# Kernel optimization log

Hardware: AMD Instinct MI355X
Metric: run time of the kernel (lower is better)

The kernel has to match this reference:

```python
import jax, jax.numpy as jnp
import numpy as np

L, B, H, P = 2048, 32, 128, 256  # seq len, batch, feature dim, state dim


def setup_inputs() -> dict:
    key = jax.random.key(0)
    ks = jax.random.split(key, 9)
    log_min, log_max = np.log(0.001), np.log(0.1)
    return {
        "input_sequences": jax.random.normal(ks[0], (L, B, H), dtype=jnp.float32),
        # -Lambda.real of a HiPPO block diag is positive; emulate with small positive values
        "log_Lambda_real": jnp.log(0.5 + jax.random.uniform(ks[1], (P,), dtype=jnp.float32)),
        "Lambda_imag": jax.random.normal(ks[2], (P,), dtype=jnp.float32) * 3.0,
        "B_tilde_r": jax.random.normal(ks[3], (P, H), dtype=jnp.float32) * (0.5 / np.sqrt(H)),
        "B_tilde_i": jax.random.normal(ks[4], (P, H), dtype=jnp.float32) * (0.5 / np.sqrt(H)),
        "C_tilde_r": jax.random.normal(ks[5], (H, P), dtype=jnp.float32) * (0.5 / np.sqrt(P)),
        "C_tilde_i": jax.random.normal(ks[6], (H, P), dtype=jnp.float32) * (0.5 / np.sqrt(P)),
        "D": jax.random.normal(ks[7], (H,), dtype=jnp.float32),
        "log_Delta": log_min + (log_max - log_min) * jax.random.uniform(ks[8], (P,), dtype=jnp.float32),
    }


def reference(input_sequences, log_Lambda_real, Lambda_imag, B_tilde_r, B_tilde_i,
              C_tilde_r, C_tilde_i, D, log_Delta):
    l = input_sequences.shape[0]
    u = input_sequences.astype(jnp.complex64)  # (L,B,H)
    lam = (-jnp.exp(log_Lambda_real) + 1j * Lambda_imag).astype(jnp.complex64)  # (P,)
    log_Lambda_bar = lam * jnp.exp(log_Delta).astype(jnp.complex64)  # scale_factor=1.0
    # kernel[t, p] = exp(log_Lambda_bar[p] * (L-1-t))  -> (L,P)
    steps = jnp.arange(l - 1, -1, -1, dtype=jnp.float32).astype(jnp.complex64)
    kernel = jnp.exp(steps[:, None] * log_Lambda_bar[None, :])
    B_tilde = (B_tilde_r + 1j * B_tilde_i).astype(jnp.complex64)  # (P,H)
    B_bar = ((kernel[-2] - 1.0) / lam)[:, None] * B_tilde  # (P,H)
    Bu = jnp.einsum('nm,lbm->lbn', B_bar, u)  # (L,B,P)
    # FFT convolution: flipped kernel is exp(log_Lambda_bar * t)
    kff = jnp.fft.fft(kernel[::-1], n=2 * l, axis=0)[:, None, :]  # (2L,1,P)
    buff = jnp.fft.fft(Bu, n=2 * l, axis=0)  # (2L,B,P)
    o = jnp.fft.ifft(kff * buff, axis=0)[:l]  # (L,B,P)
    xs = jnp.einsum('hn,lbn->lbh', (C_tilde_r + 1j * C_tilde_i).astype(jnp.complex64), o)
    xs = xs + (D * input_sequences).astype(jnp.complex64)
    return jnp.real(xs)
```

## Files before the change

kernel.cpp:

```cpp
#include <hip/hip_runtime.h>
#include <math.h>

#define SL 2048
#define NB 32
#define NH 128
#define NP 256
#define NP2 512

typedef short bf16x8 __attribute__((ext_vector_type(8)));
typedef float f32x4  __attribute__((ext_vector_type(4)));

static __device__ __forceinline__ unsigned short f2bf(float x) {
    unsigned u = __float_as_uint(x);
    return (unsigned short)((u + 0x7fffu + ((u >> 16) & 1u)) >> 16);
}
static __device__ __forceinline__ float bf2f(unsigned short h) {
    return __uint_as_float(((unsigned)h) << 16);
}
static __device__ __forceinline__ void discretize(
    const float* __restrict__ logLr, const float* __restrict__ Lim,
    const float* __restrict__ logDt, int p, float& wr, float& wi)
{
    const float Lr = expf(logLr[p]);
    const float dt = expf(logDt[p]);
    const float ew = expf(-Lr * dt);
    const float ang = Lim[p] * dt;
    wr = ew * cosf(ang); wi = ew * sinf(ang);
}

__global__ __launch_bounds__(256) void k0(
    const float* __restrict__ logLr, const float* __restrict__ Lim,
    const float* __restrict__ logDt,
    const float* __restrict__ Br, const float* __restrict__ Bi,
    const float* __restrict__ Cr, const float* __restrict__ Ci,
    unsigned short* __restrict__ BhatF, unsigned short* __restrict__ ChatF)
{
    const int tid = blockIdx.x * 256 + threadIdx.x;
    const int p = tid >> 7, h = tid & 127;
    float wr, wi; discretize(logLr, Lim, logDt, p, wr, wi);
    const float Lr = expf(logLr[p]), li = Lim[p];
    const float nr = wr - 1.0f, ni = wi;
    const float den = Lr * Lr + li * li;
    const float fr = (-nr * Lr + ni * li) / den;
    const float fi = (-ni * Lr - nr * li) / den;
    const float br = Br[p * NH + h], bi = Bi[p * NH + h];
    BhatF[((size_t)(h >> 5) << 14) + ((2 * p)     << 5) + (h & 31)] = f2bf(fr * br - fi * bi);
    BhatF[((size_t)(h >> 5) << 14) + ((2 * p + 1) << 5) + (h & 31)] = f2bf(fr * bi + fi * br);
    const int col0 = 2 * p, col1 = 2 * p + 1;
    ChatF[((size_t)(col0 >> 5) << 12) + (h << 5) + (col0 & 31)] = f2bf(Cr[h * NP + p]);
    ChatF[((size_t)(col1 >> 5) << 12) + (h << 5) + (col1 & 31)] = f2bf(-Ci[h * NP + p]);
}

__global__ __launch_bounds__(256, 4) void gA(
    const float* __restrict__ u, const unsigned short* __restrict__ BhatF,
    const float* __restrict__ logLr, const float* __restrict__ Lim,
    const float* __restrict__ logDt, float2* __restrict__ part)
{
    __shared__ unsigned short us[32][136];
    __shared__ unsigned xs[32 * 129];

    const int m  = blockIdx.x;
    const int ph = blockIdx.y;
    const int b  = blockIdx.z;
    const int tid = threadIdx.x;
    const int w = tid >> 6, lane = tid & 63;
    const int q = lane >> 4, c = lane & 15;
    const int pbase = ph * 256 + w * 64;
    const int l0 = m * 32;

    {
        const int lrow = tid >> 3;
        const int hcol = (tid & 7) * 16;
        const float* up = u + (size_t)(l0 + lrow) * (NB * NH) + b * NH + hcol;
        float4 a = *(const float4*)(up + 0);
        float4 d = *(const float4*)(up + 4);
        float4 e = *(const float4*)(up + 8);
        float4 g = *(const float4*)(up + 12);
        uint4 w0, w1;
        w0.x = (unsigned)f2bf(a.x) | ((unsigned)f2bf(a.y) << 16);
        w0.y = (unsigned)f2bf(a.z) | ((unsigned)f2bf(a.w) << 16);
        w0.z = (unsigned)f2bf(d.x) | ((unsigned)f2bf(d.y) << 16);
        w0.w = (unsigned)f2bf(d.z) | ((unsigned)f2bf(d.w) << 16);
        w1.x = (unsigned)f2bf(e.x) | ((unsigned)f2bf(e.y) << 16);
        w1.y = (unsigned)f2bf(e.z) | ((unsigned)f2bf(e.w) << 16);
        w1.z = (unsigned)f2bf(g.x) | ((unsigned)f2bf(g.y) << 16);
        w1.w = (unsigned)f2bf(g.z) | ((unsigned)f2bf(g.w) << 16);
        *(uint4*)&us[lrow][hcol + 0] = w0;
        *(uint4*)&us[lrow][hcol + 8] = w1;
    }
    __syncthreads();

    f32x4 acc[4][2];
    #pragma unroll
    for (int mt = 0; mt < 4; ++mt)
        #pragma unroll
        for (int nt = 0; nt < 2; ++nt) acc[mt][nt] = (f32x4){0.f, 0.f, 0.f, 0.f};

    #pragma unroll
    for (int kk = 0; kk < 4; ++kk) {
        bf16x8 af[4];
        #pragma unroll
        for (int mt = 0; mt < 4; ++mt)
            af[mt] = *(const bf16x8*)(BhatF + ((size_t)kk << 14)
                                      + ((pbase + 16 * mt + c) << 5) + 8 * q);
        bf16x8 bfr[2];
        #pragma unroll
        for (int nt = 0; nt < 2; ++nt)
            bfr[nt] = *(const bf16x8*)&us[16 * nt + c][kk * 32 + 8 * q];
        #pragma unroll
        for (int mt = 0; mt < 4; ++mt)
            #pragma unroll
            for (int nt = 0; nt < 2; ++nt)
                acc[mt][nt] = __builtin_amdgcn_mfma_f32_16x16x32_bf16(
                    af[mt], bfr[nt], acc[mt][nt], 0, 0, 0);
    }

    #pragma unroll
    for (int mt = 0; mt < 4; ++mt)
        #pragma unroll
        for (int nt = 0; nt < 2; ++nt) {
            const int rw  = 16 * nt + c;
            const int ppl = w * 64 + 16 * mt + 4 * q;
            ushort4 st;
            st.x = f2bf(acc[mt][nt][0]); st.y = f2bf(acc[mt][nt][1]);
            st.z = f2bf(acc[mt][nt][2]); st.w = f2bf(acc[mt][nt][3]);
            const int col = (ppl >> 1);
            xs[rw * 129 + col]     = (unsigned)st.x | ((unsigned)st.y << 16);
            xs[rw * 129 + col + 1] = (unsigned)st.z | ((unsigned)st.w << 16);
        }
    __syncthreads();

    if (tid < 128) {
        float wr, wi; discretize(logLr, Lim, logDt, ph * 128 + tid, wr, wi);
        float sr = 0.f, si = 0.f;
        unsigned va[8], vb[8];
        #pragma unroll
        for (int j = 0; j < 8; ++j) va[j] = xs[j * 129 + tid];
        #pragma unroll
        for (int k8 = 0; k8 < 4; ++k8) {
            if (k8 < 3) {
                #pragma unroll
                for (int j = 0; j < 8; ++j) vb[j] = xs[((k8 + 1) * 8 + j) * 129 + tid];
            }
            #pragma unroll
            for (int j = 0; j < 8; ++j) {
                const float xr = bf2f((unsigned short)(va[j] & 0xffffu));
                const float xi = bf2f((unsigned short)(va[j] >> 16));
                const float tr = wr * sr - wi * si + xr;
                const float ti = wr * si + wi * sr + xi;
                sr = tr; si = ti;
            }
            #pragma unroll
            for (int j = 0; j < 8; ++j) va[j] = vb[j];
        }
        part[((size_t)b * 64 + m) * NP + ph * 128 + tid] = make_float2(sr, si);
    }
}

__global__ __launch_bounds__(256) void s2(
    float2* __restrict__ part, const float* __restrict__ logLr,
    const float* __restrict__ Lim, const float* __restrict__ logDt)
{
    const int b = blockIdx.x, p = threadIdx.x;
    float wr, wi; discretize(logLr, Lim, logDt, p, wr, wi);
    float Wr = wr, Wi = wi;
    #pragma unroll
    for (int t = 0; t < 5; ++t) { const float r = Wr * Wr - Wi * Wi; Wi = 2.f * Wr * Wi; Wr = r; }
    const size_t base = (size_t)b * 64 * NP + p;
    float sr = 0.f, si = 0.f;
    float2 va[8], vb[8];
    #pragma unroll
    for (int j = 0; j < 8; ++j) va[j] = part[base + (size_t)j * NP];
    #pragma unroll
    for (int k8 = 0; k8 < 8; ++k8) {
        if (k8 < 7) {
            #pragma unroll
            for (int j = 0; j < 8; ++j)
                vb[j] = part[base + (size_t)((k8 + 1) * 8 + j) * NP];
        }
        #pragma unroll
        for (int j = 0; j < 8; ++j) {
            part[base + (size_t)(k8 * 8 + j) * NP] = make_float2(sr, si);
            const float tr = Wr * sr - Wi * si + va[j].x;
            const float ti = Wr * si + Wi * sr + va[j].y;
            sr = tr; si = ti;
        }
        #pragma unroll
        for (int j = 0; j < 8; ++j) va[j] = vb[j];
    }
}

__global__ __launch_bounds__(256, 4) void gF(
    const float* __restrict__ u, const unsigned short* __restrict__ BhatF,
    const unsigned short* __restrict__ ChatF,
    const float* __restrict__ logLr, const float* __restrict__ Lim,
    const float* __restrict__ logDt, const float2* __restrict__ Ent,
    const float* __restrict__ Dv, float* __restrict__ out)
{
    __shared__ unsigned short us[32][136];
    __shared__ char osb[16384];

    const int m = blockIdx.x, b = blockIdx.y;
    const int tid = threadIdx.x;
    const int w = tid >> 6, lane = tid & 63;
    const int q = lane >> 4, c = lane & 15;
    const int hbase = w * 32;
    const int l0 = m * 32;

    {
        const int lrow = tid >> 3;
        const int hcol = (tid & 7) * 16;
        const float* up = u + (size_t)(l0 + lrow) * (NB * NH) + b * NH + hcol;
        float4 a = *(const float4*)(up + 0);
        float4 d = *(const float4*)(up + 4);
        float4 e = *(const float4*)(up + 8);
        float4 g = *(const float4*)(up + 12);
        uint4 w0, w1;
        w0.x = (unsigned)f2bf(a.x) | ((unsigned)f2bf(a.y) << 16);
        w0.y = (unsigned)f2bf(a.z) | ((unsigned)f2bf(a.w) << 16);
        w0.z = (unsigned)f2bf(d.x) | ((unsigned)f2bf(d.y) << 16);
        w0.w = (unsigned)f2bf(d.z) | ((unsigned)f2bf(d.w) << 16);
        w1.x = (unsigned)f2bf(e.x) | ((unsigned)f2bf(e.y) << 16);
        w1.y = (unsigned)f2bf(e.z) | ((unsigned)f2bf(e.w) << 16);
        w1.z = (unsigned)f2bf(g.x) | ((unsigned)f2bf(g.y) << 16);
        w1.w = (unsigned)f2bf(g.z) | ((unsigned)f2bf(g.w) << 16);
        *(uint4*)&us[lrow][hcol + 0] = w0;
        *(uint4*)&us[lrow][hcol + 8] = w1;
    }
    __syncthreads();

    f32x4 acc2[2][2];
    #pragma unroll
    for (int mt = 0; mt < 2; ++mt)
        #pragma unroll
        for (int nt = 0; nt < 2; ++nt) acc2[mt][nt] = (f32x4){0.f, 0.f, 0.f, 0.f};

    #pragma unroll 1
    for (int half = 0; half < 2; ++half) {
        const int pbase = half * 256 + w * 64;
        f32x4 acc[4][2];
        #pragma unroll
        for (int mt = 0; mt < 4; ++mt)
            #pragma unroll
            for (int nt = 0; nt < 2; ++nt) acc[mt][nt] = (f32x4){0.f, 0.f, 0.f, 0.f};
        #pragma unroll
        for (int kk = 0; kk < 4; ++kk) {
            bf16x8 af[4];
            #pragma unroll
            for (int mt = 0; mt < 4; ++mt)
                af[mt] = *(const bf16x8*)(BhatF + ((size_t)kk << 14)
                                          + ((pbase + 16 * mt + c) << 5) + 8 * q);
            bf16x8 bfr[2];
            #pragma unroll
            for (int nt = 0; nt < 2; ++nt)
                bfr[nt] = *(const bf16x8*)&us[16 * nt + c][kk * 32 + 8 * q];
            #pragma unroll
            for (int mt = 0; mt < 4; ++mt)
                #pragma unroll
                for (int nt = 0; nt < 2; ++nt)
                    acc[mt][nt] = __builtin_amdgcn_mfma_f32_16x16x32_bf16(
                        af[mt], bfr[nt], acc[mt][nt], 0, 0, 0);
        }

        #pragma unroll
        for (int mt = 0; mt < 4; ++mt)
            #pragma unroll
            for (int nt = 0; nt < 2; ++nt) {
                const int row  = 16 * nt + c;
                const int col2 = w * 32 + 8 * mt + 2 * q;
                ushort4 st;
                st.x = f2bf(acc[mt][nt][0]); st.y = f2bf(acc[mt][nt][1]);
                st.z = f2bf(acc[mt][nt][2]); st.w = f2bf(acc[mt][nt][3]);
                const unsigned byte = (((unsigned)row << 9)
                                       + (((unsigned)col2 << 2)
                                          ^ (((unsigned)(row & 7)) << 4)));
                uint2 st2 = { (unsigned)st.x | ((unsigned)st.y << 16),
                              (unsigned)st.z | ((unsigned)st.w << 16) };
                *(uint2*)(osb + byte) = st2;
            }
        __syncthreads();

        if (tid < 128) {
            const int p = half * 128 + tid;
            float wr, wi; discretize(logLr, Lim, logDt, p, wr, wi);
            const float2 E = Ent[((size_t)(b * 64 + m)) * NP + p];
            float sr = E.x, si = E.y;
            unsigned va[32];
            #pragma unroll
            for (int j = 0; j < 32; ++j) {
                const unsigned byte = (((unsigned)j << 9)
                                       + (((unsigned)tid << 2)
                                          ^ (((unsigned)(j & 7)) << 4)));
                va[j] = *(const unsigned*)(osb + byte);
            }
            #pragma unroll
            for (int j = 0; j < 32; ++j) {
                const float xr = bf2f((unsigned short)(va[j] & 0xffffu));
                const float xi = bf2f((unsigned short)(va[j] >> 16));
                const float tr = wr * sr - wi * si + xr;
                const float ti = wr * si + wi * sr + xi;
                sr = tr; si = ti;
                va[j] = (unsigned)f2bf(tr) | ((unsigned)f2bf(ti) << 16);
            }
            #pragma unroll
            for (int j = 0; j < 32; ++j) {
                const unsigned byte = (((unsigned)j << 9)
                                       + (((unsigned)tid << 2)
                                          ^ (((unsigned)(j & 7)) << 4)));
                *(unsigned*)(osb + byte) = va[j];
            }
        }
        __syncthreads();

        #pragma unroll 4
        for (int kl = 0; kl < 8; ++kl) {
            const int kk = half * 8 + kl;
            bf16x8 af2[2];
            #pragma unroll
            for (int mt = 0; mt < 2; ++mt)
                af2[mt] = *(const bf16x8*)(ChatF + ((size_t)kk << 12)
                                           + ((hbase + (mt << 4) + c) << 5) + (q << 3));
            bf16x8 bfr2[2];
            #pragma unroll
            for (int nt = 0; nt < 2; ++nt) {
                const int r = 16 * nt + c;
                const unsigned byte = ((((unsigned)r << 9) + ((unsigned)kl << 6)
                                        + ((unsigned)q << 4))
                                       ^ (((unsigned)(c & 7)) << 4));
                bfr2[nt] = *(const bf16x8*)(osb + byte);
            }
            #pragma unroll
            for (int mt = 0; mt < 2; ++mt)
                #pragma unroll
                for (int nt = 0; nt < 2; ++nt)
                    acc2[mt][nt] = __builtin_amdgcn_mfma_f32_16x16x32_bf16(
                        af2[mt], bfr2[nt], acc2[mt][nt], 0, 0, 0);
        }
        if (half == 0) __syncthreads();
    }

    #pragma unroll
    for (int mt = 0; mt < 2; ++mt) {
        const int h4 = hbase + 16 * mt + 4 * q;
        const float4 dd = *(const float4*)(Dv + h4);
        #pragma unroll
        for (int nt = 0; nt < 2; ++nt) {
            const int l = l0 + 16 * nt + c;
            const size_t off = ((size_t)l * NB + b) * NH + h4;
            const float4 uu = *(const float4*)(u + off);
            float4 ov;
            ov.x = acc2[mt][nt][0] + dd.x * uu.x;
            ov.y = acc2[mt][nt][1] + dd.y * uu.y;
            ov.z = acc2[mt][nt][2] + dd.z * uu.z;
            ov.w = acc2[mt][nt][3] + dd.w * uu.w;
            *(float4*)(out + off) = ov;
        }
    }
}

extern "C" void kernel_launch(void* const* d_in, const int* in_sizes, int n_in,
                              void* d_out, int out_size, void* d_ws, size_t ws_size,
                              hipStream_t stream)
{
    const float* u     = (const float*)d_in[0];
    const float* logLr = (const float*)d_in[1];
    const float* Lim   = (const float*)d_in[2];
    const float* Btr   = (const float*)d_in[3];
    const float* Bti   = (const float*)d_in[4];
    const float* Ctr   = (const float*)d_in[5];
    const float* Cti   = (const float*)d_in[6];
    const float* Dv    = (const float*)d_in[7];
    const float* logDt = (const float*)d_in[8];
    float* out = (float*)d_out;

    char* ws = (char*)d_ws;
    float2*         part = (float2*)ws;
    unsigned short* Bhat = (unsigned short*)(ws + 4194304);
    unsigned short* Chat = (unsigned short*)(ws + 4325376);

    k0<<<dim3((NP * NH) / 256), 256, 0, stream>>>(logLr, Lim, logDt,
                                                  Btr, Bti, Ctr, Cti, Bhat, Chat);
    gA<<<dim3(SL / 32, 2, NB), 256, 0, stream>>>(u, Bhat, logLr, Lim, logDt, part);
    s2<<<dim3(NB), 256, 0, stream>>>(part, logLr, Lim, logDt);
    gF<<<dim3(SL / 32, NB), 256, 0, stream>>>(u, Bhat, Chat, logLr, Lim, logDt,
                                              part, Dv, out);
}
```

Before: 168.4 us.

## Fold chunk-carry scan into final kernel, removing separate s2 launch

The separate s2 kernel, which scanned per-chunk partial states sequentially across 64 chunks with only 32 blocks, is removed. Each gF block now recomputes its own entry state by scanning the preceding m chunk carries from global memory into shared memory. This drops a low-parallelism launch and its global read-modify-write. In exchange the carry work grows quadratically in total, since later chunks re-read up to 63 carries, and gF's prologue gets longer.

```diff
diff --git a/kernel.cpp b/kernel.cpp
--- a/kernel.cpp
+++ b/kernel.cpp
@@ -157,48 +157,16 @@
     }
 }
 
-__global__ __launch_bounds__(256) void s2(
-    float2* __restrict__ part, const float* __restrict__ logLr,
-    const float* __restrict__ Lim, const float* __restrict__ logDt)
-{
-    const int b = blockIdx.x, p = threadIdx.x;
-    float wr, wi; discretize(logLr, Lim, logDt, p, wr, wi);
-    float Wr = wr, Wi = wi;
-    #pragma unroll
-    for (int t = 0; t < 5; ++t) { const float r = Wr * Wr - Wi * Wi; Wi = 2.f * Wr * Wi; Wr = r; }
-    const size_t base = (size_t)b * 64 * NP + p;
-    float sr = 0.f, si = 0.f;
-    float2 va[8], vb[8];
-    #pragma unroll
-    for (int j = 0; j < 8; ++j) va[j] = part[base + (size_t)j * NP];
-    #pragma unroll
-    for (int k8 = 0; k8 < 8; ++k8) {
-        if (k8 < 7) {
-            #pragma unroll
-            for (int j = 0; j < 8; ++j)
-                vb[j] = part[base + (size_t)((k8 + 1) * 8 + j) * NP];
-        }
-        #pragma unroll
-        for (int j = 0; j < 8; ++j) {
-            part[base + (size_t)(k8 * 8 + j) * NP] = make_float2(sr, si);
-            const float tr = Wr * sr - Wi * si + va[j].x;
-            const float ti = Wr * si + Wi * sr + va[j].y;
-            sr = tr; si = ti;
-        }
-        #pragma unroll
-        for (int j = 0; j < 8; ++j) va[j] = vb[j];
-    }
-}
-
 __global__ __launch_bounds__(256, 4) void gF(
     const float* __restrict__ u, const unsigned short* __restrict__ BhatF,
     const unsigned short* __restrict__ ChatF,
     const float* __restrict__ logLr, const float* __restrict__ Lim,
-    const float* __restrict__ logDt, const float2* __restrict__ Ent,
+    const float* __restrict__ logDt, const float2* __restrict__ carr,
     const float* __restrict__ Dv, float* __restrict__ out)
 {
     __shared__ unsigned short us[32][136];
     __shared__ char osb[16384];
+    __shared__ float2 es[NP];
 
     const int m = blockIdx.x, b = blockIdx.y;
     const int tid = threadIdx.x;
@@ -206,6 +174,35 @@
     const int q = lane >> 4, c = lane & 15;
     const int hbase = w * 32;
     const int l0 = m * 32;
+
+    {
+        float wr, wi; discretize(logLr, Lim, logDt, tid, wr, wi);
+        float Wr = wr, Wi = wi;
+        #pragma unroll
+        for (int t = 0; t < 5; ++t) { const float r = Wr * Wr - Wi * Wi;
+                                      Wi = 2.f * Wr * Wi; Wr = r; }
+        float sr = 0.f, si = 0.f;
+        const float2* cp = carr + (size_t)b * 64 * NP + tid;
+        int j = 0;
+        for (; j + 8 <= m; j += 8) {
+            float2 vv[8];
+            #pragma unroll
+            for (int k = 0; k < 8; ++k) vv[k] = cp[(size_t)(j + k) * NP];
+            #pragma unroll
+            for (int k = 0; k < 8; ++k) {
+                const float tr = Wr * sr - Wi * si + vv[k].x;
+                const float ti = Wr * si + Wi * sr + vv[k].y;
+                sr = tr; si = ti;
+            }
+        }
+        for (; j < m; ++j) {
+            const float2 v = cp[(size_t)j * NP];
+            const float tr = Wr * sr - Wi * si + v.x;
+            const float ti = Wr * si + Wi * sr + v.y;
+            sr = tr; si = ti;
+        }
+        es[tid] = make_float2(sr, si);
+    }
 
     {
         const int lrow = tid >> 3;
@@ -283,7 +280,7 @@
         if (tid < 128) {
             const int p = half * 128 + tid;
             float wr, wi; discretize(logLr, Lim, logDt, p, wr, wi);
-            const float2 E = Ent[((size_t)(b * 64 + m)) * NP + p];
+            const float2 E = es[p];
             float sr = E.x, si = E.y;
             unsigned va[32];
             #pragma unroll
@@ -381,7 +378,6 @@
     k0<<<dim3((NP * NH) / 256), 256, 0, stream>>>(logLr, Lim, logDt,
                                                   Btr, Bti, Ctr, Cti, Bhat, Chat);
     gA<<<dim3(SL / 32, 2, NB), 256, 0, stream>>>(u, Bhat, logLr, Lim, logDt, part);
-    s2<<<dim3(NB), 256, 0, stream>>>(part, logLr, Lim, logDt);
     gF<<<dim3(SL / 32, NB), 256, 0, stream>>>(u, Bhat, Chat, logLr, Lim, logDt,
                                               part, Dv, out);
 }
```

After: 175.0 us. 1.04x slower.

## Fuse scan stages into one persistent kernel with grid-wide barriers

Applied to the files above, without the earlier changes.

Merges the three kernels (chunk partial scan, cross-chunk scan, final output pass) into a single persistent kernel of 1024 blocks. Each block handles two (batch, chunk) tiles, and phases are separated by atomic-counter grid barriers whose counter is zeroed by a memset before launch. This removes two kernel launches and their tail idle time. In exchange, only 32 blocks do work during the middle phase while the rest spin, and correctness requires all 1024 blocks to be co-resident, or the barrier deadlocks.

```diff
diff --git a/kernel.cpp b/kernel.cpp
--- a/kernel.cpp
+++ b/kernel.cpp
@@ -26,6 +26,19 @@
     const float ew = expf(-Lr * dt);
     const float ang = Lim[p] * dt;
     wr = ew * cosf(ang); wi = ew * sinf(ang);
+}
+
+static __device__ __forceinline__ void gbar(unsigned* __restrict__ ctr,
+                                            unsigned target) {
+    __threadfence();
+    __syncthreads();
+    if (threadIdx.x == 0) {
+        atomicAdd(ctr, 1u);
+        while (atomicAdd(ctr, 0u) < target)
+            __builtin_amdgcn_s_sleep(8);
+    }
+    __syncthreads();
+    __threadfence();
 }
 
 __global__ __launch_bounds__(256) void k0(
@@ -51,309 +64,312 @@
     ChatF[((size_t)(col1 >> 5) << 12) + (h << 5) + (col1 & 31)] = f2bf(-Ci[h * NP + p]);
 }
 
-__global__ __launch_bounds__(256, 4) void gA(
+__global__ __launch_bounds__(256, 4) void gAll(
     const float* __restrict__ u, const unsigned short* __restrict__ BhatF,
+    const unsigned short* __restrict__ ChatF,
     const float* __restrict__ logLr, const float* __restrict__ Lim,
-    const float* __restrict__ logDt, float2* __restrict__ part)
+    const float* __restrict__ logDt, float2* __restrict__ part,
+    const float* __restrict__ Dv, float* __restrict__ out,
+    unsigned* __restrict__ bars)
 {
-    __shared__ unsigned short us[32][136];
-    __shared__ unsigned xs[32 * 129];
-
-    const int m  = blockIdx.x;
-    const int ph = blockIdx.y;
-    const int b  = blockIdx.z;
+    __shared__ __align__(16) char smem[25216];
+    unsigned short (*us)[136] = (unsigned short(*)[136])smem;
+    unsigned* xs = (unsigned*)(smem + 8704);
+    char* osb = smem + 8704;
+
     const int tid = threadIdx.x;
     const int w = tid >> 6, lane = tid & 63;
     const int q = lane >> 4, c = lane & 15;
-    const int pbase = ph * 256 + w * 64;
-    const int l0 = m * 32;
-
-    {
-        const int lrow = tid >> 3;
-        const int hcol = (tid & 7) * 16;
-        const float* up = u + (size_t)(l0 + lrow) * (NB * NH) + b * NH + hcol;
-        float4 a = *(const float4*)(up + 0);
-        float4 d = *(const float4*)(up + 4);
-        float4 e = *(const float4*)(up + 8);
-        float4 g = *(const float4*)(up + 12);
-        uint4 w0, w1;
-        w0.x = (unsigned)f2bf(a.x) | ((unsigned)f2bf(a.y) << 16);
-        w0.y = (unsigned)f2bf(a.z) | ((unsigned)f2bf(a.w) << 16);
-        w0.z = (unsigned)f2bf(d.x) | ((unsigned)f2bf(d.y) << 16);
-        w0.w = (unsigned)f2bf(d.z) | ((unsigned)f2bf(d.w) << 16);
-        w1.x = (unsigned)f2bf(e.x) | ((unsigned)f2bf(e.y) << 16);
-        w1.y = (unsigned)f2bf(e.z) | ((unsigned)f2bf(e.w) << 16);
-        w1.z = (unsigned)f2bf(g.x) | ((unsigned)f2bf(g.y) << 16);
-        w1.w = (unsigned)f2bf(g.z) | ((unsigned)f2bf(g.w) << 16);
-        *(uint4*)&us[lrow][hcol + 0] = w0;
-        *(uint4*)&us[lrow][hcol + 8] = w1;
+
+    for (int it = 0; it < 2; ++it) {
+        const int t = (int)blockIdx.x + it * 1024;
+        const int b = t >> 6, m = t & 63;
+        const int l0 = m * 32;
+
+        __syncthreads();
+        {
+            const int lrow = tid >> 3;
+            const int hcol = (tid & 7) * 16;
+            const float* up = u + (size_t)(l0 + lrow) * (NB * NH) + b * NH + hcol;
+            float4 a = *(const float4*)(up + 0);
+            float4 d = *(const float4*)(up + 4);
+            float4 e = *(const float4*)(up + 8);
+            float4 g = *(const float4*)(up + 12);
+            uint4 w0, w1;
+            w0.x = (unsigned)f2bf(a.x) | ((unsigned)f2bf(a.y) << 16);
+            w0.y = (unsigned)f2bf(a.z) | ((unsigned)f2bf(a.w) << 16);
+            w0.z = (unsigned)f2bf(d.x) | ((unsigned)f2bf(d.y) << 16);
+            w0.w = (unsigned)f2bf(d.z) | ((unsigned)f2bf(d.w) << 16);
+            w1.x = (unsigned)f2bf(e.x) | ((unsigned)f2bf(e.y) << 16);
+            w1.y = (unsigned)f2bf(e.z) | ((unsigned)f2bf(e.w) << 16);
+            w1.z = (unsigned)f2bf(g.x) | ((unsigned)f2bf(g.y) << 16);
+            w1.w = (unsigned)f2bf(g.z) | ((unsigned)f2bf(g.w) << 16);
+            *(uint4*)&us[lrow][hcol + 0] = w0;
+            *(uint4*)&us[lrow][hcol + 8] = w1;
+        }
+        __syncthreads();
+
+        #pragma unroll 1
+        for (int ph = 0; ph < 2; ++ph) {
+            const int pbase = ph * 256 + w * 64;
+
+            f32x4 acc[4][2];
+            #pragma unroll
+            for (int mt = 0; mt < 4; ++mt)
+                #pragma unroll
+                for (int nt = 0; nt < 2; ++nt) acc[mt][nt] = (f32x4){0.f, 0.f, 0.f, 0.f};
+
+            #pragma unroll
+            for (int kk = 0; kk < 4; ++kk) {
+                bf16x8 af[4];
+                #pragma unroll
+                for (int mt = 0; mt < 4; ++mt)
+                    af[mt] = *(const bf16x8*)(BhatF + ((size_t)kk << 14)
+                                              + ((pbase + 16 * mt + c) << 5) + 8 * q);
+                bf16x8 bfr[2];
+                #pragma unroll
+                for (int nt = 0; nt < 2; ++nt)
+                    bfr[nt] = *(const bf16x8*)&us[16 * nt + c][kk * 32 + 8 * q];
+                #pragma unroll
+                for (int mt = 0; mt < 4; ++mt)
+                    #pragma unroll
+                    for (int nt = 0; nt < 2; ++nt)
+                        acc[mt][nt] = __builtin_amdgcn_mfma_f32_16x16x32_bf16(
+                            af[mt], bfr[nt], acc[mt][nt], 0, 0, 0);
+            }
+
+            #pragma unroll
+            for (int mt = 0; mt < 4; ++mt)
+                #pragma unroll
+                for (int nt = 0; nt < 2; ++nt) {
+                    const int rw  = 16 * nt + c;
+                    const int ppl = w * 64 + 16 * mt + 4 * q;
+                    ushort4 st;
+                    st.x = f2bf(acc[mt][nt][0]); st.y = f2bf(acc[mt][nt][1]);
+                    st.z = f2bf(acc[mt][nt][2]); st.w = f2bf(acc[mt][nt][3]);
+                    const int col = (ppl >> 1);
+                    xs[rw * 129 + col]     = (unsigned)st.x | ((unsigned)st.y << 16);
+                    xs[rw * 129 + col + 1] = (unsigned)st.z | ((unsigned)st.w << 16);
+                }
+            __syncthreads();
+
+            if (tid < 128) {
+                float wr, wi; discretize(logLr, Lim, logDt, ph * 128 + tid, wr, wi);
+                float sr = 0.f, si = 0.f;
+                unsigned va[8], vb[8];
+                #pragma unroll
+                for (int j = 0; j < 8; ++j) va[j] = xs[j * 129 + tid];
+                #pragma unroll
+                for (int k8 = 0; k8 < 4; ++k8) {
+                    if (k8 < 3) {
+                        #pragma unroll
+                        for (int j = 0; j < 8; ++j) vb[j] = xs[((k8 + 1) * 8 + j) * 129 + tid];
+                    }
+                    #pragma unroll
+                    for (int j = 0; j < 8; ++j) {
+                        const float xr = bf2f((unsigned short)(va[j] & 0xffffu));
+                        const float xi = bf2f((unsigned short)(va[j] >> 16));
+                        const float tr = wr * sr - wi * si + xr;
+                        const float ti = wr * si + wi * sr + xi;
+                        sr = tr; si = ti;
+                    }
+                    #pragma unroll
+                    for (int j = 0; j < 8; ++j) va[j] = vb[j];
+                }
+                part[((size_t)b * 64 + m) * NP + ph * 128 + tid] = make_float2(sr, si);
+            }
+            __syncthreads();
+        }
     }
-    __syncthreads();
-
-    f32x4 acc[4][2];
-    #pragma unroll
-    for (int mt = 0; mt < 4; ++mt)
+    gbar(bars + 0, 1024u);
+
+    if (blockIdx.x < NB) {
+        const int b = blockIdx.x, p = tid;
+        float wr, wi; discretize(logLr, Lim, logDt, p, wr, wi);
+        float Wr = wr, Wi = wi;
         #pragma unroll
-        for (int nt = 0; nt < 2; ++nt) acc[mt][nt] = (f32x4){0.f, 0.f, 0.f, 0.f};
-
-    #pragma unroll
-    for (int kk = 0; kk < 4; ++kk) {
-        bf16x8 af[4];
+        for (int t = 0; t < 5; ++t) { const float r = Wr * Wr - Wi * Wi;
+                                      Wi = 2.f * Wr * Wi; Wr = r; }
+        const size_t base = (size_t)b * 64 * NP + p;
+        float sr = 0.f, si = 0.f;
+        float2 va[8], vb[8];
         #pragma unroll
-        for (int mt = 0; mt < 4; ++mt)
-            af[mt] = *(const bf16x8*)(BhatF + ((size_t)kk << 14)
-                                      + ((pbase + 16 * mt + c) << 5) + 8 * q);
-        bf16x8 bfr[2];
+        for (int j = 0; j < 8; ++j) va[j] = part[base + (size_t)j * NP];
         #pragma unroll
-        for (int nt = 0; nt < 2; ++nt)
-            bfr[nt] = *(const bf16x8*)&us[16 * nt + c][kk * 32 + 8 * q];
+        for (int k8 = 0; k8 < 8; ++k8) {
+            if (k8 < 7) {
+                #pragma unroll
+                for (int j = 0; j < 8; ++j)
+                    vb[j] = part[base + (size_t)((k8 + 1) * 8 + j) * NP];
+            }
+            #pragma unroll
+            for (int j = 0; j < 8; ++j) {
+                part[base + (size_t)(k8 * 8 + j) * NP] = make_float2(sr, si);
+                const float tr = Wr * sr - Wi * si + va[j].x;
+                const float ti = Wr * si + Wi * sr + va[j].y;
+                sr = tr; si = ti;
+            }
+            #pragma unroll
+            for (int j = 0; j < 8; ++j) va[j] = vb[j];
+        }
+    }
+    gbar(bars + 16, 1024u);
+
+    for (int it = 0; it < 2; ++it) {
+        const int t = (int)blockIdx.x + it * 1024;
+        const int b = t >> 6, m = t & 63;
+        const int l0 = m * 32;
+        const int hbase = w * 32;
+
+        __syncthreads();
+        {
+            const int lrow = tid >> 3;
+            const int hcol = (tid & 7) * 16;
+            const float* up = u + (size_t)(l0 + lrow) * (NB * NH) + b * NH + hcol;
+            float4 a = *(const float4*)(up + 0);
+            float4 d = *(const float4*)(up + 4);
+            float4 e = *(const float4*)(up + 8);
+            float4 g = *(const float4*)(up + 12);
+            uint4 w0, w1;
+            w0.x = (unsigned)f2bf(a.x) | ((unsigned)f2bf(a.y) << 16);
+            w0.y = (unsigned)f2bf(a.z) | ((unsigned)f2bf(a.w) << 16);
+            w0.z = (unsigned)f2bf(d.x) | ((unsigned)f2bf(d.y) << 16);
+            w0.w = (unsigned)f2bf(d.z) | ((unsigned)f2bf(d.w) << 16);
+            w1.x = (unsigned)f2bf(e.x) | ((unsigned)f2bf(e.y) << 16);
+            w1.y = (unsigned)f2bf(e.z) | ((unsigned)f2bf(e.w) << 16);
+            w1.z = (unsigned)f2bf(g.x) | ((unsigned)f2bf(g.y) << 16);
+            w1.w = (unsigned)f2bf(g.z) | ((unsigned)f2bf(g.w) << 16);
+            *(uint4*)&us[lrow][hcol + 0] = w0;
+            *(uint4*)&us[lrow][hcol + 8] = w1;
+        }
+        __syncthreads();
+
+        f32x4 acc2[2][2];
         #pragma unroll
-        for (int mt = 0; mt < 4; ++mt)
-            #pragma unroll
-            for (int nt = 0; nt < 2; ++nt)
-                acc[mt][nt] = __builtin_amdgcn_mfma_f32_16x16x32_bf16(
-                    af[mt], bfr[nt], acc[mt][nt], 0, 0, 0);
-    }
-
-    #pragma unroll
-    for (int mt = 0; mt < 4; ++mt)
+        for (int mt = 0; mt < 2; ++mt)
+            #pragma unroll
+            for (int nt = 0; nt < 2; ++nt) acc2[mt][nt] = (f32x4){0.f, 0.f, 0.f, 0.f};
+
+        #pragma unroll 1
+        for (int half = 0; half < 2; ++half) {
+            const int pbase = half * 256 + w * 64;
+            f32x4 acc[4][2];
+            #pragma unroll
+            for (int mt = 0; mt < 4; ++mt)
+                #pragma unroll
+                for (int nt = 0; nt < 2; ++nt) acc[mt][nt] = (f32x4){0.f, 0.f, 0.f, 0.f};
+            #pragma unroll
+            for (int kk = 0; kk < 4; ++kk) {
+                bf16x8 af[4];
+                #pragma unroll
+                for (int mt = 0; mt < 4; ++mt)
+                    af[mt] = *(const bf16x8*)(BhatF + ((size_t)kk << 14)
+                                              + ((pbase + 16 * mt + c) << 5) + 8 * q);
+                bf16x8 bfr[2];
+                #pragma unroll
+                for (int nt = 0; nt < 2; ++nt)
+                    bfr[nt] = *(const bf16x8*)&us[16 * nt + c][kk * 32 + 8 * q];
+                #pragma unroll
+                for (int mt = 0; mt < 4; ++mt)
+                    #pragma unroll
+                    for (int nt = 0; nt < 2; ++nt)
+                        acc[mt][nt] = __builtin_amdgcn_mfma_f32_16x16x32_bf16(
+                            af[mt], bfr[nt], acc[mt][nt], 0, 0, 0);
+            }
+
+            #pragma unroll
+            for (int mt = 0; mt < 4; ++mt)
+                #pragma unroll
+                for (int nt = 0; nt < 2; ++nt) {
+                    const int row  = 16 * nt + c;
+                    const int col2 = w * 32 + 8 * mt + 2 * q;
+                    ushort4 st;
+                    st.x = f2bf(acc[mt][nt][0]); st.y = f2bf(acc[mt][nt][1]);
+                    st.z = f2bf(acc[mt][nt][2]); st.w = f2bf(acc[mt][nt][3]);
+                    const unsigned byte = (((unsigned)row << 9)
+                                           + (((unsigned)col2 << 2)
+                                              ^ (((unsigned)(row & 7)) << 4)));
+                    uint2 st2 = { (unsigned)st.x | ((unsigned)st.y << 16),
+                                  (unsigned)st.z | ((unsigned)st.w << 16) };
+                    *(uint2*)(osb + byte) = st2;
+                }
+            __syncthreads();
+
+            if (tid < 128) {
+                const int p = half * 128 + tid;
+                float wr, wi; discretize(logLr, Lim, logDt, p, wr, wi);
+                const float2 E = part[((size_t)(b * 64 + m)) * NP + p];
+                float sr = E.x, si = E.y;
+                unsigned va[32];
+                #pragma unroll
+                for (int j = 0; j < 32; ++j) {
+                    const unsigned byte = (((unsigned)j << 9)
+                                           + (((unsigned)tid << 2)
+                                              ^ (((unsigned)(j & 7)) << 4)));
+                    va[j] = *(const unsigned*)(osb + byte);
+                }
+                #pragma unroll
+                for (int j = 0; j < 32; ++j) {
+                    const float xr = bf2f((unsigned short)(va[j] & 0xffffu));
+                    const float xi = bf2f((unsigned short)(va[j] >> 16));
+                    const float tr = wr * sr - wi * si + xr;
+                    const float ti = wr * si + wi * sr + xi;
+                    sr = tr; si = ti;
+                    va[j] = (unsigned)f2bf(tr) | ((unsigned)f2bf(ti) << 16);
+                }
+                #pragma unroll
+                for (int j = 0; j < 32; ++j) {
+                    const unsigned byte = (((unsigned)j << 9)
+                                           + (((unsigned)tid << 2)
+                                              ^ (((unsigned)(j & 7)) << 4)));
+                    *(unsigned*)(osb + byte) = va[j];
+                }
+            }
+            __syncthreads();
+
+            #pragma unroll 4
+            for (int kl = 0; kl < 8; ++kl) {
+                const int kk = half * 8 + kl;
+                bf16x8 af2[2];
+                #pragma unroll
+                for (int mt = 0; mt < 2; ++mt)
+                    af2[mt] = *(const bf16x8*)(ChatF + ((size_t)kk << 12)
+                                               + ((hbase + (mt << 4) + c) << 5) + (q << 3));
+                bf16x8 bfr2[2];
+                #pragma unroll
+                for (int nt = 0; nt < 2; ++nt) {
+                    const int r = 16 * nt + c;
+                    const unsigned byte = ((((unsigned)r << 9) + ((unsigned)kl << 6)
+                                            + ((unsigned)q << 4))
+                                           ^ (((unsigned)(c & 7)) << 4));
+                    bfr2[nt] = *(const bf16x8*)(osb + byte);
+                }
+                #pragma unroll
+                for (int mt = 0; mt < 2; ++mt)
+                    #pragma unroll
+                    for (int nt = 0; nt < 2; ++nt)
+                        acc2[mt][nt] = __builtin_amdgcn_mfma_f32_16x16x32_bf16(
+                            af2[mt], bfr2[nt], acc2[mt][nt], 0, 0, 0);
+            }
+            if (half == 0) __syncthreads();
+        }
+
         #pragma unroll
-        for (int nt = 0; nt < 2; ++nt) {
-            const int rw  = 16 * nt + c;
-            const int ppl = w * 64 + 16 * mt + 4 * q;
-            ushort4 st;
-            st.x = f2bf(acc[mt][nt][0]); st.y = f2bf(acc[mt][nt][1]);
-            st.z = f2bf(acc[mt][nt][2]); st.w = f2bf(acc[mt][nt][3]);
-            const int col = (ppl >> 1);
-            xs[rw * 129 + col]     = (unsigned)st.x | ((unsigned)st.y << 16);
-            xs[rw * 129 + col + 1] = (unsigned)st.z | ((unsigned)st.w << 16);
-        }
-    __syncthreads();
-
-    if (tid < 128) {
-        float wr, wi; discretize(logLr, Lim, logDt, ph * 128 + tid, wr, wi);
-        float sr = 0.f, si = 0.f;
-        unsigned va[8], vb[8];
-        #pragma unroll
-        for (int j = 0; j < 8; ++j) va[j] = xs[j * 129 + tid];
-        #pragma unroll
-        for (int k8 = 0; k8 < 4; ++k8) {
-            if (k8 < 3) {
-                #pragma unroll
-                for (int j = 0; j < 8; ++j) vb[j] = xs[((k8 + 1) * 8 + j) * 129 + tid];
-            }
-            #pragma unroll
-            for (int j = 0; j < 8; ++j) {
-                const float xr = bf2f((unsigned short)(va[j] & 0xffffu));
-                const float xi = bf2f((unsigned short)(va[j] >> 16));
-                const float tr = wr * sr - wi * si + xr;
-                const float ti = wr * si + wi * sr + xi;
-                sr = tr; si = ti;
-            }
-            #pragma unroll
-            for (int j = 0; j < 8; ++j) va[j] = vb[j];
-        }
-        part[((size_t)b * 64 + m) * NP + ph * 128 + tid] = make_float2(sr, si);
-    }
-}
-
-__global__ __launch_bounds__(256) void s2(
-    float2* __restrict__ part, const float* __restrict__ logLr,
-    const float* __restrict__ Lim, const float* __restrict__ logDt)
-{
-    const int b = blockIdx.x, p = threadIdx.x;
-    float wr, wi; discretize(logLr, Lim, logDt, p, wr, wi);
-    float Wr = wr, Wi = wi;
-    #pragma unroll
-    for (int t = 0; t < 5; ++t) { const float r = Wr * Wr - Wi * Wi; Wi = 2.f * Wr * Wi; Wr = r; }
-    const size_t base = (size_t)b * 64 * NP + p;
-    float sr = 0.f, si = 0.f;
-    float2 va[8], vb[8];
-    #pragma unroll
-    for (int j = 0; j < 8; ++j) va[j] = part[base + (size_t)j * NP];
-    #pragma unroll
-    for (int k8 = 0; k8 < 8; ++k8) {
-        if (k8 < 7) {
-            #pragma unroll
-            for (int j = 0; j < 8; ++j)
-                vb[j] = part[base + (size_t)((k8 + 1) * 8 + j) * NP];
-        }
-        #pragma unroll
-        for (int j = 0; j < 8; ++j) {
-            part[base + (size_t)(k8 * 8 + j) * NP] = make_float2(sr, si);
-            const float tr = Wr * sr - Wi * si + va[j].x;
-            const float ti = Wr * si + Wi * sr + va[j].y;
-            sr = tr; si = ti;
-        }
-        #pragma unroll
-        for (int j = 0; j < 8; ++j) va[j] = vb[j];
-    }
-}
-
-__global__ __launch_bounds__(256, 4) void gF(
-    const float* __restrict__ u, const unsigned short* __restrict__ BhatF,
-    const unsigned short* __restrict__ ChatF,
-    const float* __restrict__ logLr, const float* __restrict__ Lim,
-    const float* __restrict__ logDt, const float2* __restrict__ Ent,
-    const float* __restrict__ Dv, float* __restrict__ out)
-{
-    __shared__ unsigned short us[32][136];
-    __shared__ char osb[16384];
-
-    const int m = blockIdx.x, b = blockIdx.y;
-    const int tid = threadIdx.x;
-    const int w = tid >> 6, lane = tid & 63;
-    const int q = lane >> 4, c = lane & 15;
-    const int hbase = w * 32;
-    const int l0 = m * 32;
-
-    {
-        const int lrow = tid >> 3;
-        const int hcol = (tid & 7) * 16;
-        const float* up = u + (size_t)(l0 + lrow) * (NB * NH) + b * NH + hcol;
-        float4 a = *(const float4*)(up + 0);
-        float4 d = *(const float4*)(up + 4);
-        float4 e = *(const float4*)(up + 8);
-        float4 g = *(const float4*)(up + 12);
-        uint4 w0, w1;
-        w0.x = (unsigned)f2bf(a.x) | ((unsigned)f2bf(a.y) << 16);
-        w0.y = (unsigned)f2bf(a.z) | ((unsigned)f2bf(a.w) << 16);
-        w0.z = (unsigned)f2bf(d.x) | ((unsigned)f2bf(d.y) << 16);
-        w0.w = (unsigned)f2bf(d.z) | ((unsigned)f2bf(d.w) << 16);
-        w1.x = (unsigned)f2bf(e.x) | ((unsigned)f2bf(e.y) << 16);
-        w1.y = (unsigned)f2bf(e.z) | ((unsigned)f2bf(e.w) << 16);
-        w1.z = (unsigned)f2bf(g.x) | ((unsigned)f2bf(g.y) << 16);
-        w1.w = (unsigned)f2bf(g.z) | ((unsigned)f2bf(g.w) << 16);
-        *(uint4*)&us[lrow][hcol + 0] = w0;
-        *(uint4*)&us[lrow][hcol + 8] = w1;
-    }
-    __syncthreads();
-
-    f32x4 acc2[2][2];
-    #pragma unroll
-    for (int mt = 0; mt < 2; ++mt)
-        #pragma unroll
-        for (int nt = 0; nt < 2; ++nt) acc2[mt][nt] = (f32x4){0.f, 0.f, 0.f, 0.f};
-
-    #pragma unroll 1
-    for (int half = 0; half < 2; ++half) {
-        const int pbase = half * 256 + w * 64;
-        f32x4 acc[4][2];
-        #pragma unroll
-        for (int mt = 0; mt < 4; ++mt)
-            #pragma unroll
-            for (int nt = 0; nt < 2; ++nt) acc[mt][nt] = (f32x4){0.f, 0.f, 0.f, 0.f};
-        #pragma unroll
-        for (int kk = 0; kk < 4; ++kk) {
-            bf16x8 af[4];
-            #pragma unroll
-            for (int mt = 0; mt < 4; ++mt)
-                af[mt] = *(const bf16x8*)(BhatF + ((size_t)kk << 14)
-                                          + ((pbase + 16 * mt + c) << 5) + 8 * q);
-            bf16x8 bfr[2];
-            #pragma unroll
-            for (int nt = 0; nt < 2; ++nt)
-                bfr[nt] = *(const bf16x8*)&us[16 * nt + c][kk * 32 + 8 * q];
-            #pragma unroll
-            for (int mt = 0; mt < 4; ++mt)
-                #pragma unroll
-                for (int nt = 0; nt < 2; ++nt)
-                    acc[mt][nt] = __builtin_amdgcn_mfma_f32_16x16x32_bf16(
-                        af[mt], bfr[nt], acc[mt][nt], 0, 0, 0);
-        }
-
-        #pragma unroll
-        for (int mt = 0; mt < 4; ++mt)
+        for (int mt = 0; mt < 2; ++mt) {
+            const int h4 = hbase + 16 * mt + 4 * q;
+            const float4 dd = *(const float4*)(Dv + h4);
             #pragma unroll
             for (int nt = 0; nt < 2; ++nt) {
-                const int row  = 16 * nt + c;
-                const int col2 = w * 32 + 8 * mt + 2 * q;
-                ushort4 st;
-                st.x = f2bf(acc[mt][nt][0]); st.y = f2bf(acc[mt][nt][1]);
-                st.z = f2bf(acc[mt][nt][2]); st.w = f2bf(acc[mt][nt][3]);
-                const unsigned byte = (((unsigned)row << 9)
-                                       + (((unsigned)col2 << 2)
-                                          ^ (((unsigned)(row & 7)) << 4)));
-                uint2 st2 = { (unsigned)st.x | ((unsigned)st.y << 16),
-                              (unsigned)st.z | ((unsigned)st.w << 16) };
-                *(uint2*)(osb + byte) = st2;
-            }
-        __syncthreads();
-
-        if (tid < 128) {
-            const int p = half * 128 + tid;
-            float wr, wi; discretize(logLr, Lim, logDt, p, wr, wi);
-            const float2 E = Ent[((size_t)(b * 64 + m)) * NP + p];
-            float sr = E.x, si = E.y;
-            unsigned va[32];
-            #pragma unroll
-            for (int j = 0; j < 32; ++j) {
-                const unsigned byte = (((unsigned)j << 9)
-                                       + (((unsigned)tid << 2)
-                                          ^ (((unsigned)(j & 7)) << 4)));
-                va[j] = *(const unsigned*)(osb + byte);
-            }
-            #pragma unroll
-            for (int j = 0; j < 32; ++j) {
-                const float xr = bf2f((unsigned short)(va[j] & 0xffffu));
-                const float xi = bf2f((unsigned short)(va[j] >> 16));
-                const float tr = wr * sr - wi * si + xr;
-                const float ti = wr * si + wi * sr + xi;
-                sr = tr; si = ti;
-                va[j] = (unsigned)f2bf(tr) | ((unsigned)f2bf(ti) << 16);
-            }
-            #pragma unroll
-            for (int j = 0; j < 32; ++j) {
-                const unsigned byte = (((unsigned)j << 9)
-                                       + (((unsigned)tid << 2)
-                                          ^ (((unsigned)(j & 7)) << 4)));
-                *(unsigned*)(osb + byte) = va[j];
-            }
-        }
-        __syncthreads();
-
-        #pragma unroll 4
-        for (int kl = 0; kl < 8; ++kl) {
-            const int kk = half * 8 + kl;
-            bf16x8 af2[2];
-            #pragma unroll
-            for (int mt = 0; mt < 2; ++mt)
-                af2[mt] = *(const bf16x8*)(ChatF + ((size_t)kk << 12)
-                                           + ((hbase + (mt << 4) + c) << 5) + (q << 3));
-            bf16x8 bfr2[2];
-            #pragma unroll
-            for (int nt = 0; nt < 2; ++nt) {
-                const int r = 16 * nt + c;
-                const unsigned byte = ((((unsigned)r << 9) + ((unsigned)kl << 6)
-                                        + ((unsigned)q << 4))
-                                       ^ (((unsigned)(c & 7)) << 4));
-                bfr2[nt] = *(const bf16x8*)(osb + byte);
-            }
-            #pragma unroll
-            for (int mt = 0; mt < 2; ++mt)
-                #pragma unroll
-                for (int nt = 0; nt < 2; ++nt)
-                    acc2[mt][nt] = __builtin_amdgcn_mfma_f32_16x16x32_bf16(
-                        af2[mt], bfr2[nt], acc2[mt][nt], 0, 0, 0);
-        }
-        if (half == 0) __syncthreads();
-    }
-
-    #pragma unroll
-    for (int mt = 0; mt < 2; ++mt) {
-        const int h4 = hbase + 16 * mt + 4 * q;
-        const float4 dd = *(const float4*)(Dv + h4);
-        #pragma unroll
-        for (int nt = 0; nt < 2; ++nt) {
-            const int l = l0 + 16 * nt + c;
-            const size_t off = ((size_t)l * NB + b) * NH + h4;
-            const float4 uu = *(const float4*)(u + off);
-            float4 ov;
-            ov.x = acc2[mt][nt][0] + dd.x * uu.x;
-            ov.y = acc2[mt][nt][1] + dd.y * uu.y;
-            ov.z = acc2[mt][nt][2] + dd.z * uu.z;
-            ov.w = acc2[mt][nt][3] + dd.w * uu.w;
-            *(float4*)(out + off) = ov;
+                const int l = l0 + 16 * nt + c;
+                const size_t off = ((size_t)l * NB + b) * NH + h4;
+                const float4 uu = *(const float4*)(u + off);
+                float4 ov;
+                ov.x = acc2[mt][nt][0] + dd.x * uu.x;
+                ov.y = acc2[mt][nt][1] + dd.y * uu.y;
+                ov.z = acc2[mt][nt][2] + dd.z * uu.z;
+                ov.w = acc2[mt][nt][3] + dd.w * uu.w;
+                *(float4*)(out + off) = ov;
+            }
         }
     }
 }
@@ -377,11 +393,11 @@
     float2*         part = (float2*)ws;
     unsigned short* Bhat = (unsigned short*)(ws + 4194304);
     unsigned short* Chat = (unsigned short*)(ws + 4325376);
-
+    unsigned*       bars = (unsigned*)(ws + 4456448);
+
+    hipMemsetAsync(bars, 0, 128, stream);
     k0<<<dim3((NP * NH) / 256), 256, 0, stream>>>(logLr, Lim, logDt,
                                                   Btr, Bti, Ctr, Cti, Bhat, Chat);
-    gA<<<dim3(SL / 32, 2, NB), 256, 0, stream>>>(u, Bhat, logLr, Lim, logDt, part);
-    s2<<<dim3(NB), 256, 0, stream>>>(part, logLr, Lim, logDt);
-    gF<<<dim3(SL / 32, NB), 256, 0, stream>>>(u, Bhat, Chat, logLr, Lim, logDt,
-                                              part, Dv, out);
-}
+    gAll<<<dim3(1024), 256, 0, stream>>>(u, Bhat, Chat, logLr, Lim, logDt,
+                                         part, Dv, out, bars);
+}
```

Result: slower. 539.3 us (+220.3%).
